# Kernel tuning notes

Hardware: AMD Instinct MI355X
Metric: run time of the kernel (lower is better)

Reference implementation:

```python
import jax, jax.numpy as jnp
import numpy as np


def silu(x):
    return x * jax.nn.sigmoid(x)


def setup_inputs() -> dict:
    key = jax.random.key(0)
    ks = jax.random.split(key, 12)
    B, S, Dm = 2, 2048, 768
    I, N, R, K = 1536, 16, 48, 4
    s = 0.02
    return {
        "input_states": jax.random.normal(ks[0], (B, S, Dm), jnp.float32),
        "in_proj_w": jax.random.normal(ks[1], (2 * I, Dm), jnp.float32) * s,
        "conv_w": jax.random.normal(ks[2], (I, 1, K), jnp.float32) * s,
        "conv_b": jax.random.normal(ks[3], (I,), jnp.float32) * s,
        "x_proj_w": jax.random.normal(ks[4], (R + 2 * N, I), jnp.float32) * s,
        "dt_proj_w": jax.random.normal(ks[5], (I, R), jnp.float32) * s,
        "dt_proj_b": jax.random.normal(ks[6], (I,), jnp.float32) * s,
        "A_log": jax.random.normal(ks[7], (I, N), jnp.float32) * 0.5,
        "D": jax.random.normal(ks[8], (I,), jnp.float32) * s,
        "out_proj_w": jax.random.normal(ks[9], (Dm, I), jnp.float32) * s,
        "alpha": jax.random.uniform(ks[10], (I,), jnp.float32),
        "feature_gating": jax.random.uniform(ks[11], (I,), jnp.float32),
    }


def reference(input_states, in_proj_w, conv_w, conv_b, x_proj_w,
              dt_proj_w, dt_proj_b, A_log, D, out_proj_w,
              alpha, feature_gating):
    Bsz, S, _ = input_states.shape
    I, N = A_log.shape
    R = dt_proj_w.shape[1]
    K = conv_w.shape[-1]

    # in_proj (no bias), chunk into hidden / gate, each [B, I, S]
    proj = jnp.einsum('bsd,ed->bse', input_states, in_proj_w)  # [B, S, 2I]
    hidden, gate = jnp.split(proj.transpose(0, 2, 1), 2, axis=1)

    # causal depthwise conv1d + SiLU
    h = jax.lax.conv_general_dilated(
        hidden, conv_w, window_strides=(1,), padding=[(K - 1, 0)],
        dimension_numbers=('NCH', 'OIH', 'NCH'), feature_group_count=I)
    h = silu(h + conv_b[None, :, None])  # [B, I, S]

    # x_proj -> time_step, B, C
    ssm_p = jnp.einsum('bis,ei->bse', h, x_proj_w)  # [B, S, R+2N]
    ts, Bm, Cm = jnp.split(ssm_p, [R, R + N], axis=-1)

    dt = jax.nn.softplus(jnp.einsum('bsr,ir->bsi', ts, dt_proj_w) + dt_proj_b)
    dt = dt.transpose(0, 2, 1)                       # [B, I, S]
    dt = dt.at[:, :, -1].multiply(alpha[None, :])    # alpha scales last step

    A = -jnp.exp(A_log.astype(jnp.float32))          # [I, N]
    dA = jnp.exp(A[None, :, None, :] * dt[:, :, :, None])       # [B, I, S, N]
    dBu = dt[:, :, :, None] * Bm[:, None, :, :] * h[:, :, :, None]  # [B, I, S, N]

    def step(state, xs):
        dA_t, dBu_t, C_t = xs
        state = dA_t * state + dBu_t                 # [B, I, N]
        y = jnp.einsum('bin,bn->bi', state, C_t)
        return state, y

    init = jnp.zeros((Bsz, I, N), input_states.dtype)
    _, ys = jax.lax.scan(
        step, init,
        (dA.transpose(2, 0, 1, 3), dBu.transpose(2, 0, 1, 3), Cm.transpose(1, 0, 2)))
    y = ys.transpose(1, 2, 0)                        # [B, I, S]

    y = (y + h * D[None, :, None]) * silu(gate)
    y = y.at[:, :, -1].multiply(feature_gating[None, :])
    return jnp.einsum('bis,di->bsd', y, out_proj_w)  # [B, S, Dm]
```

## Files before the change

### kernel.cpp

```cpp
#include <hip/hip_runtime.h>
#include <math.h>


static constexpr int S_LEN  = 2048;
static constexpr int DMODEL = 768;
static constexpr int ICH    = 1536;
static constexpr int NST    = 16;
static constexpr int MROWS  = 4096;
static constexpr int NCH    = 64;
static constexpr int CHS    = 32;
static constexpr int CSTR   = 2 * ICH * NST;

typedef _Float16 f16;
typedef f16 f16x8 __attribute__((ext_vector_type(8)));
typedef f16 f16x4 __attribute__((ext_vector_type(4)));
typedef f16 f16x2 __attribute__((ext_vector_type(2)));
typedef float f32x4 __attribute__((ext_vector_type(4)));

#if __has_builtin(__builtin_amdgcn_exp2f)
#define EXP2F(x) __builtin_amdgcn_exp2f(x)
#else
#define EXP2F(x) exp2f(x)
#endif

typedef __attribute__((address_space(3))) void lds_void;
typedef const __attribute__((address_space(1))) void glb_void;

__device__ __forceinline__ void glds16(f16* l, const f16* g) {
    __builtin_amdgcn_global_load_lds((glb_void*)g, (lds_void*)l, 16, 0, 0);
}

__device__ __forceinline__ float silu_f(float x) {
    return x / (1.0f + __expf(-x));
}

__global__ __launch_bounds__(256) void prep(
    const float* __restrict__ s0, f16* __restrict__ d0, int n0,
    const float* __restrict__ s1, f16* __restrict__ d1, int n1,
    float* __restrict__ z)
{
    int i = (blockIdx.x * 256 + threadIdx.x) * 4;
    if (i < n0) {
        float4 v = *(const float4*)(s0 + i);
        f16x4 o = { (f16)v.x, (f16)v.y, (f16)v.z, (f16)v.w };
        *(f16x4*)(d0 + i) = o;
    } else if (i < n0 + n1) {
        int j = i - n0;
        float4 v = *(const float4*)(s1 + j);
        f16x4 o = { (f16)v.x, (f16)v.y, (f16)v.z, (f16)v.w };
        *(f16x4*)(d1 + j) = o;
    } else {
        int j = i - n0 - n1;
        float4 zv = {};
        *(float4*)(z + j) = zv;
    }
}

__global__ __launch_bounds__(256) void k1m(
    const f16* __restrict__ Xh,
    const f16* __restrict__ Wh,
    f16* __restrict__ hidden,
    f16* __restrict__ sgate)
{
    __shared__ __align__(16) f16 As[2][128 * 32];
    __shared__ __align__(16) f16 Bs[2][64 * 32];
    const int tid = threadIdx.x;
    const int lane = tid & 63, wave = tid >> 6;
    const int quad = lane >> 4, l16 = lane & 15;
    const int wm = wave & 1, wn = wave >> 1;
    const int m0 = blockIdx.x * 128, n0 = blockIdx.y * 64;
    const int l_row = lane >> 2, l_c8 = (lane & 3) * 8;

    const f16* Ag = Xh + (size_t)(m0 + wave * 16 + l_row) * 768 + l_c8;
    const f16* Bg = Wh + (size_t)(n0 + wave * 16 + l_row) * 768 + l_c8;
    const int aLo = (wave * 16) * 32, aHi = (64 + wave * 16) * 32;
    const int bOff = (wave * 16) * 32;

#define K1_STAGE(buf, kk)                                        \
    do {                                                         \
        glds16(&As[buf][aLo], Ag + (kk));                        \
        glds16(&As[buf][aHi], Ag + (size_t)64 * 768 + (kk));     \
        glds16(&Bs[buf][bOff], Bg + (kk));                       \
    } while (0)

#define K1_COMPUTE(buf)                                                        \
    do {                                                                       \
        f16x8 af[4], bf[2];                                                    \
        _Pragma("unroll")                                                      \
        for (int mi = 0; mi < 4; ++mi)                                         \
            af[mi] = *(const f16x8*)&As[buf][(wm * 64 + mi * 16 + l16) * 32 + quad * 8]; \
        _Pragma("unroll")                                                      \
        for (int ni = 0; ni < 2; ++ni)                                         \
            bf[ni] = *(const f16x8*)&Bs[buf][(wn * 32 + ni * 16 + l16) * 32 + quad * 8]; \
        _Pragma("unroll")                                                      \
        for (int mi = 0; mi < 4; ++mi)                                         \
            _Pragma("unroll")                                                  \
            for (int ni = 0; ni < 2; ++ni)                                     \
                acc[mi][ni] = __builtin_amdgcn_mfma_f32_16x16x32_f16(          \
                    af[mi], bf[ni], acc[mi][ni], 0, 0, 0);                     \
    } while (0)

    K1_STAGE(0, 0);
    __syncthreads();

    f32x4 acc[4][2] = {};
    for (int k0 = 0; k0 < 768; k0 += 64) {
        K1_STAGE(1, k0 + 32);
        K1_COMPUTE(0);
        __syncthreads();
        if (k0 + 64 < 768) K1_STAGE(0, k0 + 64);
        K1_COMPUTE(1);
        __syncthreads();
    }
#undef K1_STAGE
#undef K1_COMPUTE

    const bool isGate = (n0 >= ICH);
    f16* outp = isGate ? sgate : hidden;
    const int e0 = (isGate ? (n0 - ICH) : n0) + wn * 32 + l16;
    #pragma unroll
    for (int mi = 0; mi < 4; ++mi) {
        #pragma unroll
        for (int ni = 0; ni < 2; ++ni) {
            #pragma unroll
            for (int r = 0; r < 4; ++r) {
                int m = m0 + wm * 64 + mi * 16 + quad * 4 + r;
                int e = e0 + ni * 16;
                float v = acc[mi][ni][r];
                if (isGate) v = silu_f(v);
                outp[(size_t)m * ICH + e] = (f16)v;
            }
        }
    }
}

__global__ __launch_bounds__(256) void k3m(
    const f16* __restrict__ hidden,
    const float* __restrict__ conv_w,
    const float* __restrict__ conv_b,
    const float* __restrict__ xw,
    f16* __restrict__ h,
    float* __restrict__ ssmp)
{
    __shared__ __align__(16) f16 Ah[128 * 32];
    __shared__ __align__(16) f16 Bh[80 * 32];
    __shared__ float4 cwv[96];
    __shared__ float  cbv[96];
    const int tid = threadIdx.x;
    const int lane = tid & 63, wave = tid >> 6;
    const int quad = lane >> 4, l16 = lane & 15;
    const int m0 = blockIdx.x * 128;
    const int kbeg = blockIdx.y * 96;

    if (tid < 96) {
        cwv[tid] = *(const float4*)(conv_w + (size_t)(kbeg + tid) * 4);
        cbv[tid] = conv_b[kbeg + tid];
    }

    f32x4 acc[2][5] = {};
    for (int k0 = kbeg; k0 < kbeg + 96; k0 += 32) {
        __syncthreads();
        #pragma unroll
        for (int it = 0; it < 2; ++it) {
            int slot = tid + it * 256;
            int r_ = slot >> 2, c_ = (slot & 3) * 8;
            int gm = m0 + r_, c = k0 + c_;
            int s = gm & (S_LEN - 1);
            const f16* bp = hidden + (size_t)gm * ICH + c;
            f16x8 x0 = *(const f16x8*)bp;
            f16x8 x1 = *(const f16x8*)(bp - (s >= 1 ? ICH : 0));
            f16x8 x2 = *(const f16x8*)(bp - (s >= 2 ? 2 * ICH : 0));
            f16x8 x3 = *(const f16x8*)(bp - (s >= 3 ? 3 * ICH : 0));
            f16x8 o;
            #pragma unroll
            for (int j = 0; j < 8; ++j) {
                int ci = (k0 - kbeg) + c_ + j;
                float4 w = cwv[ci];
                float v1 = (s >= 1) ? (float)x1[j] : 0.f;
                float v2 = (s >= 2) ? (float)x2[j] : 0.f;
                float v3 = (s >= 3) ? (float)x3[j] : 0.f;
                float r = cbv[ci] + w.x * v3 + w.y * v2 + w.z * v1 + w.w * (float)x0[j];
                o[j] = (f16)silu_f(r);
            }
            *(f16x8*)&Ah[r_ * 32 + c_] = o;
            *(f16x8*)(h + (size_t)gm * ICH + c) = o;
        }
        {
            int c4 = (tid & 7) * 4;
            for (int r = tid >> 3; r < 80; r += 32) {
                float4 v = *(const float4*)(xw + (size_t)r * ICH + k0 + c4);
                f16x4 o = { (f16)v.x, (f16)v.y, (f16)v.z, (f16)v.w };
                *(f16x4*)&Bh[r * 32 + c4] = o;
            }
        }
        __syncthreads();
        f16x8 af[2], bf[5];
        #pragma unroll
        for (int mi = 0; mi < 2; ++mi)
            af[mi] = *(const f16x8*)&Ah[(wave * 32 + mi * 16 + l16) * 32 + quad * 8];
        #pragma unroll
        for (int j = 0; j < 5; ++j)
            bf[j] = *(const f16x8*)&Bh[(j * 16 + l16) * 32 + quad * 8];
        #pragma unroll
        for (int mi = 0; mi < 2; ++mi)
            #pragma unroll
            for (int j = 0; j < 5; ++j)
                acc[mi][j] = __builtin_amdgcn_mfma_f32_16x16x32_f16(
                    af[mi], bf[j], acc[mi][j], 0, 0, 0);
    }
    #pragma unroll
    for (int mi = 0; mi < 2; ++mi) {
        #pragma unroll
        for (int j = 0; j < 5; ++j) {
            #pragma unroll
            for (int r = 0; r < 4; ++r) {
                int m = m0 + wave * 32 + mi * 16 + quad * 4 + r;
                atomicAdd(ssmp + (size_t)m * 80 + j * 16 + l16, acc[mi][j][r]);
            }
        }
    }
}

__global__ __launch_bounds__(256) void k4m(
    const float* __restrict__ ssmp,
    const float* __restrict__ dtw,
    const float* __restrict__ dtb,
    const float* __restrict__ alpha,
    f16* __restrict__ dt)
{
    __shared__ __align__(16) f16 As[128 * 72];
    __shared__ __align__(16) f16 Bs[128 * 72];
    const int tid = threadIdx.x;
    const int lane = tid & 63, wave = tid >> 6;
    const int quad = lane >> 4, l16 = lane & 15;
    const int wm = wave & 1, wn = wave >> 1;
    const int m0 = blockIdx.x * 128, n0 = blockIdx.y * 128;
    const int srow = tid >> 1;
    const int shalf = tid & 1;

    {
        const float* sa = ssmp + (size_t)(m0 + srow) * 80 + shalf * 24;
        const float* sb = dtw + (size_t)(n0 + srow) * 48 + shalf * 24;
        f16* da = &As[srow * 72 + shalf * 24];
        f16* db = &Bs[srow * 72 + shalf * 24];
        #pragma unroll
        for (int j = 0; j < 6; ++j) {
            float4 va = *(const float4*)(sa + 4 * j);
            float4 vb = *(const float4*)(sb + 4 * j);
            f16x4 oa = { (f16)va.x, (f16)va.y, (f16)va.z, (f16)va.w };
            f16x4 ob = { (f16)vb.x, (f16)vb.y, (f16)vb.z, (f16)vb.w };
            *(f16x4*)(da + 4 * j) = oa;
            *(f16x4*)(db + 4 * j) = ob;
        }
        if (shalf) {
            f16x8 z = {};
            *(f16x8*)&As[srow * 72 + 48] = z;
            *(f16x8*)&As[srow * 72 + 56] = z;
            *(f16x8*)&Bs[srow * 72 + 48] = z;
            *(f16x8*)&Bs[srow * 72 + 56] = z;
        }
    }
    __syncthreads();

    f32x4 acc[4][4] = {};
    #pragma unroll
    for (int ks = 0; ks < 2; ++ks) {
        f16x8 af[4], bf[4];
        #pragma unroll
        for (int mi = 0; mi < 4; ++mi)
            af[mi] = *(const f16x8*)&As[(wm * 64 + mi * 16 + l16) * 72 + ks * 32 + quad * 8];
        #pragma unroll
        for (int ni = 0; ni < 4; ++ni)
            bf[ni] = *(const f16x8*)&Bs[(wn * 64 + ni * 16 + l16) * 72 + ks * 32 + quad * 8];
        #pragma unroll
        for (int mi = 0; mi < 4; ++mi)
            #pragma unroll
            for (int ni = 0; ni < 4; ++ni)
                acc[mi][ni] = __builtin_amdgcn_mfma_f32_16x16x32_f16(
                    af[mi], bf[ni], acc[mi][ni], 0, 0, 0);
    }

    #pragma unroll
    for (int ni = 0; ni < 4; ++ni) {
        int e = n0 + wn * 64 + ni * 16 + l16;
        float bias = dtb[e];
        float al = alpha[e];
        #pragma unroll
        for (int mi = 0; mi < 4; ++mi) {
            #pragma unroll
            for (int r = 0; r < 4; ++r) {
                int m = m0 + wm * 64 + mi * 16 + quad * 4 + r;
                float x = acc[mi][ni][r] + bias;
                float sp = (x > 20.0f) ? x : __logf(1.0f + __expf(x));
                if ((m & (S_LEN - 1)) == S_LEN - 1) sp *= al;
                dt[(size_t)m * ICH + e] = (f16)sp;
            }
        }
    }
}

__global__ __launch_bounds__(256) void k5a_chunk(
    const f16* __restrict__ dt,
    const f16* __restrict__ h,
    const float* __restrict__ ssmp,
    const float* __restrict__ A_log,
    float* __restrict__ PArr,
    float* __restrict__ SfArr)
{
    __shared__ float dts[CHS * 64];
    __shared__ float hs[CHS * 64];
    __shared__ float Bc[CHS][16];
    const int tid = threadIdx.x;
    const int n4 = tid & 3;
    const int il = tid >> 2;
    const int i0 = blockIdx.x * 64;
    const int i = i0 + il;
    const int c = blockIdx.y;
    const int b = blockIdx.z;
    const int s0 = c * CHS;
    const size_t row0 = (size_t)(b * S_LEN + s0) * ICH + i0;

    {
        int r = tid >> 3, c8 = (tid & 7) * 8;
        size_t g_off = row0 + (size_t)r * ICH + c8;
        f16x8 dv = *(const f16x8*)(dt + g_off);
        f16x8 hv = *(const f16x8*)(h + g_off);
        #pragma unroll
        for (int j = 0; j < 8; ++j) {
            dts[r * 64 + c8 + j] = (float)dv[j];
            hs[r * 64 + c8 + j]  = (float)hv[j];
        }
    }
    if (tid < CHS * 4) {
        int t = tid >> 2, q = tid & 3;
        *(float4*)&Bc[t][q * 4] =
            *(const float4*)(ssmp + (size_t)(b * S_LEN + s0 + t) * 80 + 48 + q * 4);
    }

    const float L2E = 1.44269504088896f;
    float4 alv = *(const float4*)(A_log + i * NST + n4 * 4);
    float A[4] = { -__expf(alv.x) * L2E, -__expf(alv.y) * L2E,
                   -__expf(alv.z) * L2E, -__expf(alv.w) * L2E };
    float st[4] = {};
    float cdt = 0.f;
    __syncthreads();
    #pragma unroll 4
    for (int t = 0; t < CHS; ++t) {
        float dtv = dts[t * 64 + il];
        float hv  = hs[t * 64 + il];
        float4 Bv = *(const float4*)&Bc[t][n4 * 4];
        cdt += dtv;
        float x = dtv * hv;
        #pragma unroll
        for (int j = 0; j < 4; ++j) {
            float dA = EXP2F(A[j] * dtv);
            st[j] = fmaf(dA, st[j], x * (&Bv.x)[j]);
        }
    }
    size_t base = (size_t)c * CSTR + (size_t)(b * ICH + i) * NST + n4 * 4;
    float4 Pv = { EXP2F(A[0] * cdt), EXP2F(A[1] * cdt),
                  EXP2F(A[2] * cdt), EXP2F(A[3] * cdt) };
    float4 Sv = { st[0], st[1], st[2], st[3] };
    *(float4*)(PArr + base)  = Pv;
    *(float4*)(SfArr + base) = Sv;
}

__global__ __launch_bounds__(256) void k5b_carry(
    const float* PArr,
    const float* __restrict__ SfArr,
    float* CIn)
{
    int idx = blockIdx.x * 256 + threadIdx.x;
    float p[NCH], s[NCH];
    #pragma unroll
    for (int c = 0; c < NCH; ++c) {
        size_t a = (size_t)c * CSTR + idx;
        p[c] = PArr[a];
        s[c] = SfArr[a];
    }
    float carry = 0.f;
    #pragma unroll
    for (int c = 0; c < NCH; ++c) {
        CIn[(size_t)c * CSTR + idx] = carry;
        carry = fmaf(p[c], carry, s[c]);
    }
}

__global__ __launch_bounds__(256) void k5c_emit(
    const f16* __restrict__ dt,
    const f16* __restrict__ h,
    const f16* __restrict__ sgate,
    const float* __restrict__ ssmp,
    const float* __restrict__ A_log,
    const float* __restrict__ Dp,
    const float* __restrict__ fg,
    const float* __restrict__ CIn,
    f16* __restrict__ yh)
{
    __shared__ float dts[CHS * 64];
    __shared__ float hs[CHS * 64];
    __shared__ float gs[CHS * 64];
    __shared__ float BC[CHS][32];
    const int tid = threadIdx.x;
    const int n4 = tid & 3;
    const int il = tid >> 2;
    const int i0 = blockIdx.x * 64;
    const int i = i0 + il;
    const int c = blockIdx.y;
    const int b = blockIdx.z;
    const int s0 = c * CHS;
    const size_t row0 = (size_t)(b * S_LEN + s0) * ICH + i0;

    {
        int r = tid >> 3, c8 = (tid & 7) * 8;
        size_t g_off = row0 + (size_t)r * ICH + c8;
        f16x8 dv = *(const f16x8*)(dt + g_off);
        f16x8 hv = *(const f16x8*)(h + g_off);
        f16x8 gv = *(const f16x8*)(sgate + g_off);
        #pragma unroll
        for (int j = 0; j < 8; ++j) {
            dts[r * 64 + c8 + j] = (float)dv[j];
            hs[r * 64 + c8 + j]  = (float)hv[j];
            gs[r * 64 + c8 + j]  = (float)gv[j];
        }
    }
    {
        int t = tid >> 3, q = tid & 7;
        *(float4*)&BC[t][q * 4] =
            *(const float4*)(ssmp + (size_t)(b * S_LEN + s0 + t) * 80 + 48 + q * 4);
    }

    const float L2E = 1.44269504088896f;
    float4 alv = *(const float4*)(A_log + i * NST + n4 * 4);
    float A[4] = { -__expf(alv.x) * L2E, -__expf(alv.y) * L2E,
                   -__expf(alv.z) * L2E, -__expf(alv.w) * L2E };
    const float Dv = Dp[i];
    const float fgv = fg[i];
    float4 civ = *(const float4*)(CIn + (size_t)c * CSTR + (size_t)(b * ICH + i) * NST + n4 * 4);
    float st[4] = { civ.x, civ.y, civ.z, civ.w };
    f16* yout = yh + row0 + il;
    const bool last_chunk = (c == NCH - 1);
    __syncthreads();
    #pragma unroll 4
    for (int t = 0; t < CHS; ++t) {
        float dtv = dts[t * 64 + il];
        float hv  = hs[t * 64 + il];
        float4 Bv = *(const float4*)&BC[t][n4 * 4];
        float4 Cv = *(const float4*)&BC[t][16 + n4 * 4];
        float x = dtv * hv;
        float yp = 0.f;
        #pragma unroll
        for (int j = 0; j < 4; ++j) {
            float dA = EXP2F(A[j] * dtv);
            st[j] = fmaf(dA, st[j], x * (&Bv.x)[j]);
            yp = fmaf(st[j], (&Cv.x)[j], yp);
        }
        yp += __shfl_xor(yp, 1, 4);
        yp += __shfl_xor(yp, 2, 4);
        if (n4 == 0) {
            float yv = fmaf(hv, Dv, yp) * gs[t * 64 + il];
            if (last_chunk && t == CHS - 1) yv *= fgv;
            yout[(size_t)t * ICH] = (f16)yv;
        }
    }
}

__global__ __launch_bounds__(256) void k6m(
    const f16* __restrict__ Yh,
    const float* __restrict__ OWf,
    float* __restrict__ out)
{
    __shared__ __align__(16) f16 As[4][64 * 32];
    __shared__ __align__(16) f16 Bs[4][64 * 40];
    const int tid = threadIdx.x;
    const int lane = tid & 63, wave = tid >> 6;
    const int quad = lane >> 4, l16 = lane & 15;
    const int wm = wave & 1, wn = wave >> 1;
    const int m0 = blockIdx.x * 64, n0 = blockIdx.y * 64;
    const int l_row = lane >> 2, l_c8 = (lane & 3) * 8;

    const f16* Ag = Yh + (size_t)(m0 + wave * 16 + l_row) * ICH + l_c8;
    const int aOff = (wave * 16) * 32;
    const int brow = tid >> 2, bc8 = (tid & 3) * 8;
    const float* Bgf = OWf + (size_t)(n0 + brow) * ICH + bc8;
    float4 vb0, vb1, vb2, vb3;

#define K6_STAGEA(hb, kk) glds16(&As[hb][aOff], Ag + (kk))

#define K6_LOADB2(kk)                                            \
    do {                                                         \
        vb0 = *(const float4*)(Bgf + (kk));                      \
        vb1 = *(const float4*)(Bgf + (kk) + 4);                  \
        vb2 = *(const float4*)(Bgf + (kk) + 32);                 \
        vb3 = *(const float4*)(Bgf + (kk) + 36);                 \
    } while (0)

#define K6_WRITEB2(hb0, hb1)                                                   \
    do {                                                                       \
        f16x8 o0 = { (f16)vb0.x, (f16)vb0.y, (f16)vb0.z, (f16)vb0.w,           \
                     (f16)vb1.x, (f16)vb1.y, (f16)vb1.z, (f16)vb1.w };         \
        f16x8 o1 = { (f16)vb2.x, (f16)vb2.y, (f16)vb2.z, (f16)vb2.w,           \
                     (f16)vb3.x, (f16)vb3.y, (f16)vb3.z, (f16)vb3.w };         \
        *(f16x8*)&Bs[hb0][brow * 40 + bc8] = o0;                               \
        *(f16x8*)&Bs[hb1][brow * 40 + bc8] = o1;                               \
    } while (0)

#define K6_COMPUTE(hb)                                                         \
    do {                                                                       \
        f16x8 af[2], bf[2];                                                    \
        _Pragma("unroll")                                                      \
        for (int mi = 0; mi < 2; ++mi)                                         \
            af[mi] = *(const f16x8*)&As[hb][(wm * 32 + mi * 16 + l16) * 32 + quad * 8]; \
        _Pragma("unroll")                                                      \
        for (int ni = 0; ni < 2; ++ni)                                         \
            bf[ni] = *(const f16x8*)&Bs[hb][(wn * 32 + ni * 16 + l16) * 40 + quad * 8]; \
        _Pragma("unroll")                                                      \
        for (int mi = 0; mi < 2; ++mi)                                         \
            _Pragma("unroll")                                                  \
            for (int ni = 0; ni < 2; ++ni)                                     \
                acc[mi][ni] = __builtin_amdgcn_mfma_f32_16x16x32_f16(          \
                    af[mi], bf[ni], acc[mi][ni], 0, 0, 0);                     \
    } while (0)

    K6_STAGEA(0, 0);
    K6_STAGEA(1, 32);
    K6_LOADB2(0);
    K6_WRITEB2(0, 1);
    __syncthreads();

    f32x4 acc[2][2] = {};
    for (int h = 0; h < 48; h += 2) {
        const bool more = (h + 2 < 48);
        if (more) {
            K6_STAGEA((h + 2) & 3, (h + 2) * 32);
            K6_STAGEA((h + 3) & 3, (h + 3) * 32);
            K6_LOADB2((h + 2) * 32);
        }
        K6_COMPUTE(h & 3);
        K6_COMPUTE((h + 1) & 3);
        if (more) K6_WRITEB2((h + 2) & 3, (h + 3) & 3);
        __syncthreads();
    }
#undef K6_STAGEA
#undef K6_LOADB2
#undef K6_WRITEB2
#undef K6_COMPUTE

    #pragma unroll
    for (int mi = 0; mi < 2; ++mi) {
        #pragma unroll
        for (int ni = 0; ni < 2; ++ni) {
            #pragma unroll
            for (int r = 0; r < 4; ++r) {
                int m = m0 + wm * 32 + mi * 16 + quad * 4 + r;
                int d = n0 + wn * 32 + ni * 16 + l16;
                out[(size_t)m * DMODEL + d] = acc[mi][ni][r];
            }
        }
    }
}

extern "C" void kernel_launch(void* const* d_in, const int* in_sizes, int n_in,
                              void* d_out, int out_size, void* d_ws, size_t ws_size,
                              hipStream_t stream) {
    const float* X     = (const float*)d_in[0];
    const float* W1    = (const float*)d_in[1];
    const float* CW    = (const float*)d_in[2];
    const float* CB    = (const float*)d_in[3];
    const float* XW    = (const float*)d_in[4];
    const float* DTW   = (const float*)d_in[5];
    const float* DTB   = (const float*)d_in[6];
    const float* ALOG  = (const float*)d_in[7];
    const float* DD    = (const float*)d_in[8];
    const float* OW    = (const float*)d_in[9];
    const float* ALPHA = (const float*)d_in[10];
    const float* FG    = (const float*)d_in[11];
    float* out = (float*)d_out;

    const size_t NBI = (size_t)MROWS * ICH;
    f16* hidden_h = (f16*)d_ws;
    f16* sgate_h  = hidden_h + NBI;
    f16* h_h      = sgate_h + NBI;
    f16* dt_h     = h_h + NBI;
    float* ssmp   = (float*)(dt_h + NBI);
    f16* Xh       = (f16*)(ssmp + (size_t)MROWS * 80);
    f16* W1h      = Xh + (size_t)MROWS * DMODEL;
    float* SfA    = (float*)(W1h + (size_t)2 * ICH * DMODEL);
    float* PArr = (float*)hidden_h;
    float* CIn  = PArr;
    f16* yh     = (f16*)SfA;

    const int nX = MROWS * DMODEL;
    const int nW1 = 2 * ICH * DMODEL;
    const int nS = MROWS * 80;
    prep<<<dim3((nX + nW1 + nS) / 1024), 256, 0, stream>>>(X, Xh, nX, W1, W1h, nW1, ssmp);
    k1m<<<dim3(32, 48), 256, 0, stream>>>(Xh, W1h, hidden_h, sgate_h);
    k3m<<<dim3(32, 16), 256, 0, stream>>>(hidden_h, CW, CB, XW, h_h, ssmp);
    k4m<<<dim3(32, 12), 256, 0, stream>>>(ssmp, DTW, DTB, ALPHA, dt_h);
    k5a_chunk<<<dim3(24, NCH, 2), 256, 0, stream>>>(dt_h, h_h, ssmp, ALOG, PArr, SfA);
    k5b_carry<<<dim3(192), 256, 0, stream>>>(PArr, SfA, CIn);
    k5c_emit<<<dim3(24, NCH, 2), 256, 0, stream>>>(dt_h, h_h, sgate_h, ssmp, ALOG, DD, FG, CIn, yh);
    k6m<<<dim3(64, 12), 256, 0, stream>>>(yh, OW, out);
}
```

Measured before the change: 241.5 us.

## Fuse dt projection and softplus into scan chunk and emit kernels

Removes the separate k4m GEMM kernel that wrote dt as a [B*S, I] f16 tensor. Both scan kernels now compute their chunk's dt tile in place with a small MFMA over the time-step features and dt_proj weights, followed by softplus and alpha scaling, all in shared memory. This drops one kernel launch and a full dt write plus two reads of global memory. The cost is computing the projection twice, once per scan pass, and extra shared memory and barriers per block.

```diff
diff --git a/kernel.cpp b/kernel.cpp
--- a/kernel.cpp
+++ b/kernel.cpp
@@ -221,96 +221,26 @@
     }
 }
 
-__global__ __launch_bounds__(256) void k4m(
+__global__ __launch_bounds__(256) void k5a_chunk(
+    const f16* __restrict__ h,
     const float* __restrict__ ssmp,
+    const float* __restrict__ A_log,
     const float* __restrict__ dtw,
     const float* __restrict__ dtb,
     const float* __restrict__ alpha,
-    f16* __restrict__ dt)
+    float* __restrict__ PArr,
+    float* __restrict__ SfArr)
 {
-    __shared__ __align__(16) f16 As[128 * 72];
-    __shared__ __align__(16) f16 Bs[128 * 72];
+    __shared__ float hs[CHS * 64];
+    __shared__ float Bc[CHS][16];
+    __shared__ __align__(16) f16 stage[(CHS + 64) * 72];
+    float* dts = (float*)stage;
+    f16* ts_l = stage;
+    f16* dw_l = stage + CHS * 72;
+
     const int tid = threadIdx.x;
     const int lane = tid & 63, wave = tid >> 6;
     const int quad = lane >> 4, l16 = lane & 15;
-    const int wm = wave & 1, wn = wave >> 1;
-    const int m0 = blockIdx.x * 128, n0 = blockIdx.y * 128;
-    const int srow = tid >> 1;
-    const int shalf = tid & 1;
-
-    {
-        const float* sa = ssmp + (size_t)(m0 + srow) * 80 + shalf * 24;
-        const float* sb = dtw + (size_t)(n0 + srow) * 48 + shalf * 24;
-        f16* da = &As[srow * 72 + shalf * 24];
-        f16* db = &Bs[srow * 72 + shalf * 24];
-        #pragma unroll
-        for (int j = 0; j < 6; ++j) {
-            float4 va = *(const float4*)(sa + 4 * j);
-            float4 vb = *(const float4*)(sb + 4 * j);
-            f16x4 oa = { (f16)va.x, (f16)va.y, (f16)va.z, (f16)va.w };
-            f16x4 ob = { (f16)vb.x, (f16)vb.y, (f16)vb.z, (f16)vb.w };
-            *(f16x4*)(da + 4 * j) = oa;
-            *(f16x4*)(db + 4 * j) = ob;
-        }
-        if (shalf) {
-            f16x8 z = {};
-            *(f16x8*)&As[srow * 72 + 48] = z;
-            *(f16x8*)&As[srow * 72 + 56] = z;
-            *(f16x8*)&Bs[srow * 72 + 48] = z;
-            *(f16x8*)&Bs[srow * 72 + 56] = z;
-        }
-    }
-    __syncthreads();
-
-    f32x4 acc[4][4] = {};
-    #pragma unroll
-    for (int ks = 0; ks < 2; ++ks) {
-        f16x8 af[4], bf[4];
-        #pragma unroll
-        for (int mi = 0; mi < 4; ++mi)
-            af[mi] = *(const f16x8*)&As[(wm * 64 + mi * 16 + l16) * 72 + ks * 32 + quad * 8];
-        #pragma unroll
-        for (int ni = 0; ni < 4; ++ni)
-            bf[ni] = *(const f16x8*)&Bs[(wn * 64 + ni * 16 + l16) * 72 + ks * 32 + quad * 8];
-        #pragma unroll
-        for (int mi = 0; mi < 4; ++mi)
-            #pragma unroll
-            for (int ni = 0; ni < 4; ++ni)
-                acc[mi][ni] = __builtin_amdgcn_mfma_f32_16x16x32_f16(
-                    af[mi], bf[ni], acc[mi][ni], 0, 0, 0);
-    }
-
-    #pragma unroll
-    for (int ni = 0; ni < 4; ++ni) {
-        int e = n0 + wn * 64 + ni * 16 + l16;
-        float bias = dtb[e];
-        float al = alpha[e];
-        #pragma unroll
-        for (int mi = 0; mi < 4; ++mi) {
-            #pragma unroll
-            for (int r = 0; r < 4; ++r) {
-                int m = m0 + wm * 64 + mi * 16 + quad * 4 + r;
-                float x = acc[mi][ni][r] + bias;
-                float sp = (x > 20.0f) ? x : __logf(1.0f + __expf(x));
-                if ((m & (S_LEN - 1)) == S_LEN - 1) sp *= al;
-                dt[(size_t)m * ICH + e] = (f16)sp;
-            }
-        }
-    }
-}
-
-__global__ __launch_bounds__(256) void k5a_chunk(
-    const f16* __restrict__ dt,
-    const f16* __restrict__ h,
-    const float* __restrict__ ssmp,
-    const float* __restrict__ A_log,
-    float* __restrict__ PArr,
-    float* __restrict__ SfArr)
-{
-    __shared__ float dts[CHS * 64];
-    __shared__ float hs[CHS * 64];
-    __shared__ float Bc[CHS][16];
-    const int tid = threadIdx.x;
     const int n4 = tid & 3;
     const int il = tid >> 2;
     const int i0 = blockIdx.x * 64;
@@ -323,27 +253,72 @@
     {
         int r = tid >> 3, c8 = (tid & 7) * 8;
         size_t g_off = row0 + (size_t)r * ICH + c8;
-        f16x8 dv = *(const f16x8*)(dt + g_off);
         f16x8 hv = *(const f16x8*)(h + g_off);
         #pragma unroll
-        for (int j = 0; j < 8; ++j) {
-            dts[r * 64 + c8 + j] = (float)dv[j];
-            hs[r * 64 + c8 + j]  = (float)hv[j];
-        }
+        for (int j = 0; j < 8; ++j) hs[r * 64 + c8 + j] = (float)hv[j];
     }
     if (tid < CHS * 4) {
         int t = tid >> 2, q = tid & 3;
         *(float4*)&Bc[t][q * 4] =
             *(const float4*)(ssmp + (size_t)(b * S_LEN + s0 + t) * 80 + 48 + q * 4);
     }
+    #pragma unroll
+    for (int j = 0; j < 2; ++j) {
+        int idx = tid + j * 256;
+        if (idx < 384) {
+            int r = idx / 12, q = idx - r * 12;
+            float4 v = *(const float4*)(ssmp + (size_t)(b * S_LEN + s0 + r) * 80 + q * 4);
+            f16x4 o = { (f16)v.x, (f16)v.y, (f16)v.z, (f16)v.w };
+            *(f16x4*)&ts_l[r * 72 + q * 4] = o;
+        }
+    }
+    #pragma unroll
+    for (int j = 0; j < 3; ++j) {
+        int idx = tid + j * 256;
+        int r = idx / 12, q = idx - r * 12;
+        float4 v = *(const float4*)(dtw + (size_t)(i0 + r) * 48 + q * 4);
+        f16x4 o = { (f16)v.x, (f16)v.y, (f16)v.z, (f16)v.w };
+        *(f16x4*)&dw_l[r * 72 + q * 4] = o;
+    }
+    if (tid < 64)  { f16x8 z = {}; int r = tid >> 1, hf = tid & 1; *(f16x8*)&ts_l[r * 72 + 48 + hf * 8] = z; }
+    if (tid < 128) { f16x8 z = {}; int r = tid >> 1, hf = tid & 1; *(f16x8*)&dw_l[r * 72 + 48 + hf * 8] = z; }
 
     const float L2E = 1.44269504088896f;
     float4 alv = *(const float4*)(A_log + i * NST + n4 * 4);
     float A[4] = { -__expf(alv.x) * L2E, -__expf(alv.y) * L2E,
                    -__expf(alv.z) * L2E, -__expf(alv.w) * L2E };
+    __syncthreads();
+
+    f32x4 acc2[2] = {};
+    #pragma unroll
+    for (int ks = 0; ks < 2; ++ks) {
+        f16x8 bf = *(const f16x8*)&dw_l[(wave * 16 + l16) * 72 + ks * 32 + quad * 8];
+        #pragma unroll
+        for (int tt = 0; tt < 2; ++tt) {
+            f16x8 af = *(const f16x8*)&ts_l[(tt * 16 + l16) * 72 + ks * 32 + quad * 8];
+            acc2[tt] = __builtin_amdgcn_mfma_f32_16x16x32_f16(af, bf, acc2[tt], 0, 0, 0);
+        }
+    }
+    __syncthreads();
+    {
+        int ig = i0 + wave * 16 + l16;
+        float bias = dtb[ig];
+        #pragma unroll
+        for (int tt = 0; tt < 2; ++tt) {
+            #pragma unroll
+            for (int r = 0; r < 4; ++r) {
+                int t = tt * 16 + quad * 4 + r;
+                float x = acc2[tt][r] + bias;
+                float sp = (x > 20.0f) ? x : __logf(1.0f + __expf(x));
+                if (c == NCH - 1 && t == CHS - 1) sp *= alpha[ig];
+                dts[t * 64 + wave * 16 + l16] = sp;
+            }
+        }
+    }
+    __syncthreads();
+
     float st[4] = {};
     float cdt = 0.f;
-    __syncthreads();
     #pragma unroll 4
     for (int t = 0; t < CHS; ++t) {
         float dtv = dts[t * 64 + il];
@@ -387,21 +362,29 @@
 }
 
 __global__ __launch_bounds__(256) void k5c_emit(
-    const f16* __restrict__ dt,
     const f16* __restrict__ h,
     const f16* __restrict__ sgate,
     const float* __restrict__ ssmp,
     const float* __restrict__ A_log,
+    const float* __restrict__ dtw,
+    const float* __restrict__ dtb,
+    const float* __restrict__ alpha,
     const float* __restrict__ Dp,
     const float* __restrict__ fg,
     const float* __restrict__ CIn,
     f16* __restrict__ yh)
 {
-    __shared__ float dts[CHS * 64];
     __shared__ float hs[CHS * 64];
     __shared__ float gs[CHS * 64];
     __shared__ float BC[CHS][32];
+    __shared__ __align__(16) f16 stage[(CHS + 64) * 72];
+    float* dts = (float*)stage;
+    f16* ts_l = stage;
+    f16* dw_l = stage + CHS * 72;
+
     const int tid = threadIdx.x;
+    const int lane = tid & 63, wave = tid >> 6;
+    const int quad = lane >> 4, l16 = lane & 15;
     const int n4 = tid & 3;
     const int il = tid >> 2;
     const int i0 = blockIdx.x * 64;
@@ -414,14 +397,12 @@
     {
         int r = tid >> 3, c8 = (tid & 7) * 8;
         size_t g_off = row0 + (size_t)r * ICH + c8;
-        f16x8 dv = *(const f16x8*)(dt + g_off);
         f16x8 hv = *(const f16x8*)(h + g_off);
         f16x8 gv = *(const f16x8*)(sgate + g_off);
         #pragma unroll
         for (int j = 0; j < 8; ++j) {
-            dts[r * 64 + c8 + j] = (float)dv[j];
-            hs[r * 64 + c8 + j]  = (float)hv[j];
-            gs[r * 64 + c8 + j]  = (float)gv[j];
+            hs[r * 64 + c8 + j] = (float)hv[j];
+            gs[r * 64 + c8 + j] = (float)gv[j];
         }
     }
     {
@@ -429,6 +410,26 @@
         *(float4*)&BC[t][q * 4] =
             *(const float4*)(ssmp + (size_t)(b * S_LEN + s0 + t) * 80 + 48 + q * 4);
     }
+    #pragma unroll
+    for (int j = 0; j < 2; ++j) {
+        int idx = tid + j * 256;
+        if (idx < 384) {
+            int r = idx / 12, q = idx - r * 12;
+            float4 v = *(const float4*)(ssmp + (size_t)(b * S_LEN + s0 + r) * 80 + q * 4);
+            f16x4 o = { (f16)v.x, (f16)v.y, (f16)v.z, (f16)v.w };
+            *(f16x4*)&ts_l[r * 72 + q * 4] = o;
+        }
+    }
+    #pragma unroll
+    for (int j = 0; j < 3; ++j) {
+        int idx = tid + j * 256;
+        int r = idx / 12, q = idx - r * 12;
+        float4 v = *(const float4*)(dtw + (size_t)(i0 + r) * 48 + q * 4);
+        f16x4 o = { (f16)v.x, (f16)v.y, (f16)v.z, (f16)v.w };
+        *(f16x4*)&dw_l[r * 72 + q * 4] = o;
+    }
+    if (tid < 64)  { f16x8 z = {}; int r = tid >> 1, hf = tid & 1; *(f16x8*)&ts_l[r * 72 + 48 + hf * 8] = z; }
+    if (tid < 128) { f16x8 z = {}; int r = tid >> 1, hf = tid & 1; *(f16x8*)&dw_l[r * 72 + 48 + hf * 8] = z; }
 
     const float L2E = 1.44269504088896f;
     float4 alv = *(const float4*)(A_log + i * NST + n4 * 4);
@@ -437,10 +438,39 @@
     const float Dv = Dp[i];
     const float fgv = fg[i];
     float4 civ = *(const float4*)(CIn + (size_t)c * CSTR + (size_t)(b * ICH + i) * NST + n4 * 4);
+    __syncthreads();
+
+    f32x4 acc2[2] = {};
+    #pragma unroll
+    for (int ks = 0; ks < 2; ++ks) {
+        f16x8 bf = *(const f16x8*)&dw_l[(wave * 16 + l16) * 72 + ks * 32 + quad * 8];
+        #pragma unroll
+        for (int tt = 0; tt < 2; ++tt) {
+            f16x8 af = *(const f16x8*)&ts_l[(tt * 16 + l16) * 72 + ks * 32 + quad * 8];
+            acc2[tt] = __builtin_amdgcn_mfma_f32_16x16x32_f16(af, bf, acc2[tt], 0, 0, 0);
+        }
+    }
+    __syncthreads();
+    {
+        int ig = i0 + wave * 16 + l16;
+        float bias = dtb[ig];
+        #pragma unroll
+        for (int tt = 0; tt < 2; ++tt) {
+            #pragma unroll
+            for (int r = 0; r < 4; ++r) {
+                int t = tt * 16 + quad * 4 + r;
+                float x = acc2[tt][r] + bias;
+                float sp = (x > 20.0f) ? x : __logf(1.0f + __expf(x));
+                if (c == NCH - 1 && t == CHS - 1) sp *= alpha[ig];
+                dts[t * 64 + wave * 16 + l16] = sp;
+            }
+        }
+    }
+    __syncthreads();
+
     float st[4] = { civ.x, civ.y, civ.z, civ.w };
     f16* yout = yh + row0 + il;
     const bool last_chunk = (c == NCH - 1);
-    __syncthreads();
     #pragma unroll 4
     for (int t = 0; t < CHS; ++t) {
         float dtv = dts[t * 64 + il];
@@ -596,9 +626,8 @@
     prep<<<dim3((nX + nW1 + nS) / 1024), 256, 0, stream>>>(X, Xh, nX, W1, W1h, nW1, ssmp);
     k1m<<<dim3(32, 48), 256, 0, stream>>>(Xh, W1h, hidden_h, sgate_h);
     k3m<<<dim3(32, 16), 256, 0, stream>>>(hidden_h, CW, CB, XW, h_h, ssmp);
-    k4m<<<dim3(32, 12), 256, 0, stream>>>(ssmp, DTW, DTB, ALPHA, dt_h);
-    k5a_chunk<<<dim3(24, NCH, 2), 256, 0, stream>>>(dt_h, h_h, ssmp, ALOG, PArr, SfA);
+    k5a_chunk<<<dim3(24, NCH, 2), 256, 0, stream>>>(h_h, ssmp, ALOG, DTW, DTB, ALPHA, PArr, SfA);
     k5b_carry<<<dim3(192), 256, 0, stream>>>(PArr, SfA, CIn);
-    k5c_emit<<<dim3(24, NCH, 2), 256, 0, stream>>>(dt_h, h_h, sgate_h, ssmp, ALOG, DD, FG, CIn, yh);
+    k5c_emit<<<dim3(24, NCH, 2), 256, 0, stream>>>(h_h, sgate_h, ssmp, ALOG, DTW, DTB, ALPHA, DD, FG, CIn, yh);
     k6m<<<dim3(64, 12), 256, 0, stream>>>(yh, OW, out);
 }
```

Result: no change. 242.3 us (+0.3%).
